# Kernel tuning notes

Hardware: AMD Instinct MI355X
Metric: run time of the kernel (lower is better)

Reference implementation:

```python
import jax, jax.numpy as jnp
import numpy as np

D_K = 128
NEG_MAX = float(np.finfo(np.float32).max)  # original uses -finfo(float32).max


def setup_inputs() -> dict:
    key = jax.random.key(0)
    kq, kk, kv, km = jax.random.split(key, 4)
    B, S, D = 16, 2048, D_K
    q = jax.random.normal(kq, (B, S, D), dtype=jnp.float32)
    k = jax.random.normal(kk, (B, S, D), dtype=jnp.float32)
    v = jax.random.normal(kv, (B, S, D), dtype=jnp.float32)
    mask = jax.random.randint(km, (B, S, S), 0, 2).astype(jnp.bool_)
    return {"q": q, "k": k, "v": v, "mask": mask}


def reference(q, k, v, mask):
    # scores: [B, S, S] = q @ k^T / sqrt(d_k)
    scale = 1.0 / np.sqrt(D_K).astype(np.float32)
    scores = jnp.einsum('bqd,bkd->bqk', q, k) * scale
    scores = jnp.where(mask, -NEG_MAX, scores)  # masked_fill with -float32 max
    attn = jax.nn.softmax(scores, axis=2)
    return jnp.einsum('bqk,bkd->bqd', attn, v)
```

## Files before the change

kernel.cpp:

```cpp
#include <hip/hip_runtime.h>

#define NTHREADS 256

typedef __attribute__((ext_vector_type(8))) short bf16x8;
typedef __attribute__((ext_vector_type(4))) float f32x4;
typedef __attribute__((ext_vector_type(2))) unsigned uint2v;
typedef __attribute__((ext_vector_type(4))) unsigned uint4v;

constexpr int kB = 16, kS = 2048, kD = 128;
constexpr int QBLK = 128, KBLK = 32;
constexpr int MSTRIDE = 36;
constexpr float kNegMax = -3.402823466e38f;
constexpr float kMClamp = -1e30f;
constexpr float kDeferThr = 8.0f;

__device__ __forceinline__ unsigned cvt_pk(float lo, float hi) {
    unsigned r;
    asm("v_cvt_pk_bf16_f32 %0, %1, %2" : "=v"(r) : "v"(lo), "v"(hi));
    return r;
}

#define SWZ(bytecol, row) ((bytecol) ^ (((row) & 7) << 4))
#define KEYV(d) ((((d) & 7) ^ (((d) >> 2) & 7)) & 7)

template<int SPLIT>
__global__ __launch_bounds__(NTHREADS, 2)
void attn_fwd(const float* __restrict__ q, const float* __restrict__ k,
              const float* __restrict__ v, const int* __restrict__ mask,
              float* __restrict__ out, float* __restrict__ ws)
{
    __shared__ __align__(16) char smem[29184];
    char* K_lds  = smem;
    char* VT_lds = smem + 8192;
    char* P_lds  = smem + 16384;
    unsigned char* M_lds = (unsigned char*)(smem + 24576);

    const int tid = threadIdx.x, lane = tid & 63, w = tid >> 6;
    const int l15 = lane & 15, lg = lane >> 4;

    const int bid = (int)blockIdx.x;
    int b, qbase, kbase;
    if (SPLIT == 1) {
        int swz = (bid & 7) * 32 + (bid >> 3);
        b = swz >> 4; qbase = (swz & 15) * QBLK; kbase = 0;
    } else {
        int swz = (bid & 7) * 64 + (bid >> 3);
        b = swz >> 5;
        int rem = swz & 31;
        qbase = (rem >> 1) * QBLK;
        kbase = (rem & 1) * (kS / 2);
    }
    const int nrounds = (SPLIT == 1) ? (kS / KBLK) : (kS / KBLK / 2);

    const float scale = 0.08838834764831845f;
    bf16x8 qf[2][4];
    #pragma unroll
    for (int qs = 0; qs < 2; ++qs) {
        const float* qp = q + ((size_t)(b*kS + qbase + w*32 + qs*16 + l15)) * kD;
        #pragma unroll
        for (int kk = 0; kk < 4; ++kk) {
            float4 a = *(const float4*)(qp + kk*32 + lg*8);
            float4 c = *(const float4*)(qp + kk*32 + lg*8 + 4);
            uint4v pk = { cvt_pk(a.x*scale, a.y*scale), cvt_pk(a.z*scale, a.w*scale),
                          cvt_pk(c.x*scale, c.y*scale), cvt_pk(c.z*scale, c.w*scale) };
            qf[qs][kk] = __builtin_bit_cast(bf16x8, pk);
        }
    }

    f32x4 acc[2][8];
    #pragma unroll
    for (int qs = 0; qs < 2; ++qs)
        #pragma unroll
        for (int d = 0; d < 8; ++d) acc[qs][d] = f32x4{0.f,0.f,0.f,0.f};
    float m_r[2] = {kMClamp, kMClamp};
    float l_r[2] = {0.f, 0.f};

    const float* kbat = k + (size_t)b * kS * kD;
    const float* vbat = v + (size_t)b * kS * kD;
    const int*   mbat = mask + ((size_t)b * kS + qbase) * kS;

    char* Pw = P_lds + w * 2048;
    const int kg = tid >> 5, dg = tid & 31;

    float4 kreg[2][2];
    float4 vreg[4];
    int4   mreg[4];

    auto LOAD = [&](int kt0) {
        #pragma unroll
        for (int c = 0; c < 2; ++c) {
            int chunk = c * 256 + tid;
            int row = chunk >> 4, col8 = chunk & 15;
            const float4* ptr = (const float4*)(kbat + (size_t)(kt0 + row)*kD + col8*8);
            kreg[c][0] = ptr[0];
            kreg[c][1] = ptr[1];
        }
        #pragma unroll
        for (int r = 0; r < 4; ++r)
            vreg[r] = *(const float4*)(vbat + (size_t)(kt0 + kg*4 + r)*kD + dg*4);
        #pragma unroll
        for (int c = 0; c < 4; ++c) {
            int idx = c * 256 + tid;
            int mrow = idx >> 3, mc4 = idx & 7;
            mreg[c] = *(const int4*)(mbat + (size_t)mrow*kS + kt0 + mc4*4);
        }
    };

    auto STORE = [&]() {
        #pragma unroll
        for (int c = 0; c < 2; ++c) {
            int chunk = c * 256 + tid;
            int row = chunk >> 4, col8 = chunk & 15;
            uint4v pk = { cvt_pk(kreg[c][0].x, kreg[c][0].y), cvt_pk(kreg[c][0].z, kreg[c][0].w),
                          cvt_pk(kreg[c][1].x, kreg[c][1].y), cvt_pk(kreg[c][1].z, kreg[c][1].w) };
            *(uint4v*)(K_lds + row*256 + SWZ(col8*16, row)) = pk;
        }
        #pragma unroll
        for (int jj = 0; jj < 4; ++jj) {
            int d = dg * 4 + jj;
            int col = (d >> 6) * 64 + kg * 8;
            uint2v pk = { cvt_pk((&vreg[0].x)[jj], (&vreg[1].x)[jj]),
                          cvt_pk((&vreg[2].x)[jj], (&vreg[3].x)[jj]) };
            *(uint2v*)(VT_lds + (d & 63)*128 + (col ^ (KEYV(d) << 4))) = pk;
        }
        #pragma unroll
        for (int c = 0; c < 4; ++c) {
            int idx = c * 256 + tid;
            int mrow = idx >> 3, mc4 = idx & 7;
            unsigned pk = (unsigned)(mreg[c].x != 0)
                        | ((unsigned)(mreg[c].y != 0) << 8)
                        | ((unsigned)(mreg[c].z != 0) << 16)
                        | ((unsigned)(mreg[c].w != 0) << 24);
            *(unsigned*)(M_lds + mrow*MSTRIDE + mc4*4) = pk;
        }
    };

    LOAD(kbase);

    for (int t = 0; t < nrounds; ++t) {
        __syncthreads();
        STORE();
        __syncthreads();
        if (t + 1 < nrounds) LOAD(kbase + (t + 1) * KBLK);

        f32x4 z[2][2];
        #pragma unroll
        for (int qs = 0; qs < 2; ++qs)
            #pragma unroll
            for (int kt = 0; kt < 2; ++kt) z[qs][kt] = f32x4{0.f,0.f,0.f,0.f};
        #pragma unroll
        for (int kt = 0; kt < 2; ++kt) {
            bf16x8 kf[4];
            int krow = kt*16 + l15;
            #pragma unroll
            for (int kk = 0; kk < 4; ++kk)
                kf[kk] = *(const bf16x8*)(K_lds + krow*256 + SWZ(kk*64 + lg*16, krow));
            #pragma unroll
            for (int qs = 0; qs < 2; ++qs)
                #pragma unroll
                for (int kk = 0; kk < 4; ++kk)
                    z[qs][kt] = __builtin_amdgcn_mfma_f32_16x16x32_bf16(kf[kk], qf[qs][kk], z[qs][kt], 0, 0, 0);
        }

        #pragma unroll
        for (int qs = 0; qs < 2; ++qs) {
            const int mrowb = (w*32 + qs*16 + l15) * MSTRIDE;
            float mx = kNegMax;
            #pragma unroll
            for (int kt = 0; kt < 2; ++kt) {
                unsigned nib = *(const unsigned*)(M_lds + mrowb + kt*16 + lg*4);
                #pragma unroll
                for (int i = 0; i < 4; ++i) {
                    float sv = ((nib >> (8*i)) & 0xFFu) ? kNegMax : z[qs][kt][i];
                    z[qs][kt][i] = sv;
                    mx = fmaxf(mx, sv);
                }
            }
            mx = fmaxf(mx, __shfl_xor(mx, 16));
            mx = fmaxf(mx, __shfl_xor(mx, 32));
            if (!__all(mx <= m_r[qs] + kDeferThr)) {
                float mnew = fmaxf(m_r[qs], mx);
                float corr = __expf(m_r[qs] - mnew);
                l_r[qs] *= corr;
                #pragma unroll
                for (int d = 0; d < 8; ++d) acc[qs][d] *= corr;
                m_r[qs] = mnew;
            }
            float rs = 0.f;
            #pragma unroll
            for (int kt = 0; kt < 2; ++kt) {
                float p0 = __expf(z[qs][kt][0] - m_r[qs]);
                float p1 = __expf(z[qs][kt][1] - m_r[qs]);
                float p2 = __expf(z[qs][kt][2] - m_r[qs]);
                float p3 = __expf(z[qs][kt][3] - m_r[qs]);
                rs += (p0 + p1) + (p2 + p3);
                uint2v pk = { cvt_pk(p0, p1), cvt_pk(p2, p3) };
                int col = qs*64 + kt*32 + lg*8;
                *(uint2v*)(Pw + l15*128 + (col ^ ((l15 & 7) << 4))) = pk;
            }
            rs += __shfl_xor(rs, 16);
            rs += __shfl_xor(rs, 32);
            l_r[qs] += rs;
        }

        bf16x8 pf[2];
        #pragma unroll
        for (int qs = 0; qs < 2; ++qs) {
            int col = qs*64 + lg*16;
            pf[qs] = *(const bf16x8*)(Pw + l15*128 + (col ^ ((l15 & 7) << 4)));
        }
        #pragma unroll
        for (int dblk = 0; dblk < 8; ++dblk) {
            int d = dblk*16 + l15;
            int col = (d >> 6) * 64 + lg*16;
            bf16x8 vf = *(const bf16x8*)(VT_lds + (d & 63)*128 + (col ^ (KEYV(d) << 4)));
            #pragma unroll
            for (int qs = 0; qs < 2; ++qs)
                acc[qs][dblk] = __builtin_amdgcn_mfma_f32_16x16x32_bf16(vf, pf[qs], acc[qs][dblk], 0, 0, 0);
        }
    }

    if (SPLIT == 1) {
        #pragma unroll
        for (int qs = 0; qs < 2; ++qs) {
            float inv = 1.0f / l_r[qs];
            float* op = out + ((size_t)(b*kS + qbase + w*32 + qs*16 + l15)) * kD;
            #pragma unroll
            for (int dblk = 0; dblk < 8; ++dblk) {
                float4 r;
                r.x = acc[qs][dblk][0] * inv;
                r.y = acc[qs][dblk][1] * inv;
                r.z = acc[qs][dblk][2] * inv;
                r.w = acc[qs][dblk][3] * inv;
                *(float4*)(op + dblk*16 + lg*4) = r;
            }
        }
    } else {
        const int half = (kbase != 0);
        #pragma unroll
        for (int qs = 0; qs < 2; ++qs) {
            const size_t row = (size_t)half * (kB*kS) + (size_t)b*kS + qbase + w*32 + qs*16 + l15;
            float* op = ws + row * kD;
            #pragma unroll
            for (int dblk = 0; dblk < 8; ++dblk) {
                float4 r;
                r.x = acc[qs][dblk][0]; r.y = acc[qs][dblk][1];
                r.z = acc[qs][dblk][2]; r.w = acc[qs][dblk][3];
                *(float4*)(op + dblk*16 + lg*4) = r;
            }
            if (lg == 0) {
                float* ml = ws + (size_t)2*kB*kS*kD;
                ml[row*2 + 0] = m_r[qs];
                ml[row*2 + 1] = l_r[qs];
            }
        }
    }
}

__global__ __launch_bounds__(NTHREADS)
void attn_merge(const float* __restrict__ ws, float* __restrict__ out)
{
    const float* ml = ws + (size_t)2*kB*kS*kD;
    const int tid = threadIdx.x;
    const size_t r = (size_t)blockIdx.x * 8 + (tid >> 5);
    const int c = (tid & 31) * 4;
    float m0 = ml[r*2 + 0],               l0 = ml[r*2 + 1];
    float m1 = ml[((size_t)kB*kS + r)*2], l1 = ml[((size_t)kB*kS + r)*2 + 1];
    float mS = fmaxf(m0, m1);
    float e0 = __expf(m0 - mS), e1 = __expf(m1 - mS);
    float inv = 1.0f / (l0*e0 + l1*e1);
    float4 o0 = *(const float4*)(ws + r*kD + c);
    float4 o1 = *(const float4*)(ws + (size_t)kB*kS*kD + r*kD + c);
    float4 rr;
    rr.x = (o0.x*e0 + o1.x*e1) * inv;
    rr.y = (o0.y*e0 + o1.y*e1) * inv;
    rr.z = (o0.z*e0 + o1.z*e1) * inv;
    rr.w = (o0.w*e0 + o1.w*e1) * inv;
    *(float4*)(out + r*kD + c) = rr;
}

extern "C" void kernel_launch(void* const* d_in, const int* in_sizes, int n_in,
                              void* d_out, int out_size, void* d_ws, size_t ws_size,
                              hipStream_t stream) {
    const float* q = (const float*)d_in[0];
    const float* k = (const float*)d_in[1];
    const float* v = (const float*)d_in[2];
    const int* mask = (const int*)d_in[3];
    float* out = (float*)d_out;
    const size_t wsNeeded = (size_t)2*kB*kS*kD*4 + (size_t)2*kB*kS*2*4;
    if (ws_size >= wsNeeded) {
        attn_fwd<2><<<dim3(kB * (kS/QBLK) * 2), dim3(NTHREADS), 0, stream>>>(
            q, k, v, mask, out, (float*)d_ws);
        attn_merge<<<dim3(kB*kS/8), dim3(NTHREADS), 0, stream>>>((const float*)d_ws, out);
    } else {
        attn_fwd<1><<<dim3(kB * (kS/QBLK)), dim3(NTHREADS), 0, stream>>>(
            q, k, v, mask, out, nullptr);
    }
}
```

Baseline: 106.8 us.

## Feed P to PV MFMA straight from registers and use exp2 softmax

Drops the LDS round-trip for the probability tile P. The PV product now uses 16x16x16 bf16 MFMAs, whose operand layout matches the QK^T accumulator layout, so P stays in registers. It also folds log2(e) into the Q scale and switches exp to exp2 in both the main and merge kernels. The cost is twice as many smaller MFMA instructions and narrower V reads from LDS. LDS use also drops, which may help occupancy.

```diff
diff --git a/kernel.cpp b/kernel.cpp
--- a/kernel.cpp
+++ b/kernel.cpp
@@ -3,6 +3,7 @@
 #define NTHREADS 256
 
 typedef __attribute__((ext_vector_type(8))) short bf16x8;
+typedef __attribute__((ext_vector_type(4))) short bf16x4;
 typedef __attribute__((ext_vector_type(4))) float f32x4;
 typedef __attribute__((ext_vector_type(2))) unsigned uint2v;
 typedef __attribute__((ext_vector_type(4))) unsigned uint4v;
@@ -20,6 +21,15 @@
     return r;
 }
 
+__device__ __forceinline__ f32x4 mfma16(bf16x4 a, bf16x4 b, f32x4 c) {
+#if __has_builtin(__builtin_amdgcn_mfma_f32_16x16x16bf16_1k)
+    return __builtin_amdgcn_mfma_f32_16x16x16bf16_1k(a, b, c, 0, 0, 0);
+#else
+    asm("v_mfma_f32_16x16x16_bf16 %0, %1, %2, %0" : "+v"(c) : "v"(a), "v"(b));
+    return c;
+#endif
+}
+
 #define SWZ(bytecol, row) ((bytecol) ^ (((row) & 7) << 4))
 #define KEYV(d) ((((d) & 7) ^ (((d) >> 2) & 7)) & 7)
 
@@ -29,11 +39,10 @@
               const float* __restrict__ v, const int* __restrict__ mask,
               float* __restrict__ out, float* __restrict__ ws)
 {
-    __shared__ __align__(16) char smem[29184];
+    __shared__ __align__(16) char smem[20992];
     char* K_lds  = smem;
     char* VT_lds = smem + 8192;
-    char* P_lds  = smem + 16384;
-    unsigned char* M_lds = (unsigned char*)(smem + 24576);
+    unsigned char* M_lds = (unsigned char*)(smem + 16384);
 
     const int tid = threadIdx.x, lane = tid & 63, w = tid >> 6;
     const int l15 = lane & 15, lg = lane >> 4;
@@ -52,7 +61,7 @@
     }
     const int nrounds = (SPLIT == 1) ? (kS / KBLK) : (kS / KBLK / 2);
 
-    const float scale = 0.08838834764831845f;
+    const float scale = 0.08838834764831845f * 1.4426950408889634f;
     bf16x8 qf[2][4];
     #pragma unroll
     for (int qs = 0; qs < 2; ++qs) {
@@ -79,7 +88,6 @@
     const float* vbat = v + (size_t)b * kS * kD;
     const int*   mbat = mask + ((size_t)b * kS + qbase) * kS;
 
-    char* Pw = P_lds + w * 2048;
     const int kg = tid >> 5, dg = tid & 31;
 
     float4 kreg[2][2];
@@ -162,6 +170,7 @@
                     z[qs][kt] = __builtin_amdgcn_mfma_f32_16x16x32_bf16(kf[kk], qf[qs][kk], z[qs][kt], 0, 0, 0);
         }
 
+        bf16x4 pfA[2], pfB[2];
         #pragma unroll
         for (int qs = 0; qs < 2; ++qs) {
             const int mrowb = (w*32 + qs*16 + l15) * MSTRIDE;
@@ -180,43 +189,43 @@
             mx = fmaxf(mx, __shfl_xor(mx, 32));
             if (!__all(mx <= m_r[qs] + kDeferThr)) {
                 float mnew = fmaxf(m_r[qs], mx);
-                float corr = __expf(m_r[qs] - mnew);
+                float corr = exp2f(m_r[qs] - mnew);
                 l_r[qs] *= corr;
                 #pragma unroll
                 for (int d = 0; d < 8; ++d) acc[qs][d] *= corr;
                 m_r[qs] = mnew;
             }
-            float rs = 0.f;
-            #pragma unroll
-            for (int kt = 0; kt < 2; ++kt) {
-                float p0 = __expf(z[qs][kt][0] - m_r[qs]);
-                float p1 = __expf(z[qs][kt][1] - m_r[qs]);
-                float p2 = __expf(z[qs][kt][2] - m_r[qs]);
-                float p3 = __expf(z[qs][kt][3] - m_r[qs]);
-                rs += (p0 + p1) + (p2 + p3);
-                uint2v pk = { cvt_pk(p0, p1), cvt_pk(p2, p3) };
-                int col = qs*64 + kt*32 + lg*8;
-                *(uint2v*)(Pw + l15*128 + (col ^ ((l15 & 7) << 4))) = pk;
-            }
+            float p00 = exp2f(z[qs][0][0] - m_r[qs]);
+            float p01 = exp2f(z[qs][0][1] - m_r[qs]);
+            float p02 = exp2f(z[qs][0][2] - m_r[qs]);
+            float p03 = exp2f(z[qs][0][3] - m_r[qs]);
+            float p10 = exp2f(z[qs][1][0] - m_r[qs]);
+            float p11 = exp2f(z[qs][1][1] - m_r[qs]);
+            float p12 = exp2f(z[qs][1][2] - m_r[qs]);
+            float p13 = exp2f(z[qs][1][3] - m_r[qs]);
+            float rs = ((p00 + p01) + (p02 + p03)) + ((p10 + p11) + (p12 + p13));
             rs += __shfl_xor(rs, 16);
             rs += __shfl_xor(rs, 32);
             l_r[qs] += rs;
-        }
-
-        bf16x8 pf[2];
-        #pragma unroll
-        for (int qs = 0; qs < 2; ++qs) {
-            int col = qs*64 + lg*16;
-            pf[qs] = *(const bf16x8*)(Pw + l15*128 + (col ^ ((l15 & 7) << 4)));
-        }
+            uint2v pa = { cvt_pk(p00, p01), cvt_pk(p02, p03) };
+            uint2v pb = { cvt_pk(p10, p11), cvt_pk(p12, p13) };
+            pfA[qs] = __builtin_bit_cast(bf16x4, pa);
+            pfB[qs] = __builtin_bit_cast(bf16x4, pb);
+        }
+
         #pragma unroll
         for (int dblk = 0; dblk < 8; ++dblk) {
             int d = dblk*16 + l15;
-            int col = (d >> 6) * 64 + lg*16;
-            bf16x8 vf = *(const bf16x8*)(VT_lds + (d & 63)*128 + (col ^ (KEYV(d) << 4)));
-            #pragma unroll
-            for (int qs = 0; qs < 2; ++qs)
-                acc[qs][dblk] = __builtin_amdgcn_mfma_f32_16x16x32_bf16(vf, pf[qs], acc[qs][dblk], 0, 0, 0);
+            int rowb = (d & 63) * 128;
+            int half = (d >> 6) * 64;
+            int key = KEYV(d) << 4;
+            bf16x4 vf0 = *(const bf16x4*)(VT_lds + rowb + ((half + lg*8) ^ key));
+            bf16x4 vf1 = *(const bf16x4*)(VT_lds + rowb + ((half + 32 + lg*8) ^ key));
+            #pragma unroll
+            for (int qs = 0; qs < 2; ++qs) {
+                acc[qs][dblk] = mfma16(vf0, pfA[qs], acc[qs][dblk]);
+                acc[qs][dblk] = mfma16(vf1, pfB[qs], acc[qs][dblk]);
+            }
         }
     }
 
@@ -267,7 +276,7 @@
     float m0 = ml[r*2 + 0],               l0 = ml[r*2 + 1];
     float m1 = ml[((size_t)kB*kS + r)*2], l1 = ml[((size_t)kB*kS + r)*2 + 1];
     float mS = fmaxf(m0, m1);
-    float e0 = __expf(m0 - mS), e1 = __expf(m1 - mS);
+    float e0 = exp2f(m0 - mS), e1 = exp2f(m1 - mS);
     float inv = 1.0f / (l0*e0 + l1*e1);
     float4 o0 = *(const float4*)(ws + r*kD + c);
     float4 o1 = *(const float4*)(ws + (size_t)kB*kS*kD + r*kD + c);
```

Result: no change. 107.2 us, median of 4 (+0.4%).
